# Performance work log

Hardware: AMD Instinct MI355X
Metric: run time of the kernel (lower is better)

## Reference

```python
import jax, jax.numpy as jnp
import numpy as np

LAYERS = [2, 1024, 512, 256, 128, 1]
LB = jnp.array([0.0, 0.0], dtype=jnp.float32)
UB = jnp.array([2.0 * np.pi, 1.0], dtype=jnp.float32)


def _block_diag_mask(num_blocks, bs1, bs2):
    return jnp.kron(jnp.eye(num_blocks, dtype=jnp.float32), jnp.ones((bs1, bs2), jnp.float32))


def _masks():
    # masks for l in range(2, num_Layers - 2) with num_Layers = len(LAYERS) = 6 -> l in {2, 3}
    width = [LAYERS[0]] + [(2 ** (i - 1)) * LAYERS[i] for i in range(1, len(LAYERS) - 1)] + [LAYERS[-1]]
    masks = []
    for l in range(2, len(LAYERS) - 2):
        num_blocks = 2 ** (l - 1)
        bs1 = width[l] // num_blocks
        bs2 = 2 * LAYERS[l + 1]
        masks.append(_block_diag_mask(num_blocks, bs1, bs2))
    return masks


def setup_inputs() -> dict:
    key = jax.random.key(0)
    ks = jax.random.split(key, 8)
    N = 65536
    H = 1024

    def xavier(k, fi, fo):
        lim = float(np.sqrt(6.0 / (fi + fo)))
        return jax.random.uniform(k, (fi, fo), jnp.float32, -lim, lim)

    X = jax.random.uniform(ks[0], (N, 2), jnp.float32, 0.0, 1.0) * (UB - LB) + LB
    return {
        "X": X,
        "W0": xavier(ks[1], 2, H), "b0": jnp.zeros((1, H), jnp.float32),
        "W1": xavier(ks[2], H, H), "b1": jnp.zeros((1, H), jnp.float32),
        "W2": xavier(ks[3], H, H), "b2": jnp.zeros((1, H), jnp.float32),
        "W3": xavier(ks[4], H, H), "b3": jnp.zeros((1, H), jnp.float32),
        "W_last": xavier(ks[5], H, 1), "b_last": jnp.zeros((1, 1), jnp.float32),
    }


def reference(X, W0, b0, W1, b1, W2, b2, W3, b3, W_last, b_last):
    mask2, mask3 = _masks()
    # input normalization to [-1, 1]
    h = 2.0 * (X - LB) / (UB - LB) - 1.0
    h = jnp.tanh(h @ W0 + b0)                 # layer 0: dense
    h = jnp.tanh(h @ W1 + b1)                 # layer 1: dense (no mask in forward)
    h = jnp.tanh(h @ (W2 * mask2) + b2)       # layer 2: block-diagonal masked
    h = jnp.tanh(h @ (W3 * mask3) + b3)       # layer 3: block-diagonal masked
    return h @ W_last + b_last                # output layer, [N, 1]
```

## Files before the change

### kernel.cpp

```cpp
#include <hip/hip_runtime.h>
#include <cstdint>
#include <cstddef>


typedef _Float16  f16x8   __attribute__((ext_vector_type(8)));
typedef float     floatx4 __attribute__((ext_vector_type(4)));
typedef float     floatx8 __attribute__((ext_vector_type(8)));

__device__ __forceinline__ float tanh_fast(float x) {
    float e = __expf(2.0f * x);
    return 1.0f - 2.0f / (e + 1.0f);
}

__global__ __launch_bounds__(256)
void transposeH(const float* __restrict__ W, _Float16* __restrict__ Wt) {
    __shared__ float tile[32][33];
    const int tx = threadIdx.x & 31;
    const int ty = threadIdx.x >> 5;
    #pragma unroll
    for (int j = 0; j < 4; ++j) {
        int r = ty + j * 8;
        tile[r][tx] = W[(size_t)(blockIdx.y * 32 + r) * 1024 + blockIdx.x * 32 + tx];
    }
    __syncthreads();
    #pragma unroll
    for (int j = 0; j < 4; ++j) {
        int r = ty + j * 8;
        Wt[(size_t)(blockIdx.x * 32 + r) * 1024 + blockIdx.y * 32 + tx] =
            (_Float16)tile[tx][r];
    }
}

__global__ __launch_bounds__(256)
void layer0_kernel(const float* __restrict__ X, const float* __restrict__ W0,
                   const float* __restrict__ b0, _Float16* __restrict__ H) {
    const int idx = blockIdx.x * 256 + threadIdx.x;
    const int row = idx >> 7;
    const int j0  = (idx & 127) << 3;
    const float x0 = X[row * 2 + 0];
    const float x1 = X[row * 2 + 1];
    const float xa = x0 * 0.31830988618379067f - 1.0f;
    const float xb = 2.0f * x1 - 1.0f;
    floatx8 wa = *(const floatx8*)(W0 + j0);
    floatx8 wb = *(const floatx8*)(W0 + 1024 + j0);
    floatx8 bb = *(const floatx8*)(b0 + j0);
    f16x8 o;
    #pragma unroll
    for (int j = 0; j < 8; ++j) {
        float v = fmaf(xa, wa[j], fmaf(xb, wb[j], bb[j]));
        o[j] = (_Float16)tanh_fast(v);
    }
    *(f16x8*)(H + (size_t)row * 1024 + j0) = o;
}

__global__ __launch_bounds__(256)
void gemm_tanh_f16(const _Float16* __restrict__ A, const _Float16* __restrict__ Bt,
                   const float* __restrict__ bias, _Float16* __restrict__ C, int KB) {
    __shared__ _Float16 As[128 * 32];
    __shared__ _Float16 Bs[128 * 32];

    const int tid  = threadIdx.x;
    const int lane = tid & 63;
    const int wave = tid >> 6;
    const int m0 = blockIdx.x * 128;
    const int n0 = blockIdx.y * 128;
    const int kbeg   = (n0 / KB) * KB;
    const int kiters = KB >> 5;
    const int wm = (wave & 1) << 6;
    const int wn = (wave >> 1) << 6;
    const int r = lane & 15;
    const int q = lane >> 4;

    const int rowS0 = tid >> 2;
    const int rowS1 = 64 + rowS0;
    const int seg   = (tid & 3) << 3;
    const size_t gA0 = (size_t)(m0 + rowS0) * 1024 + kbeg + seg;
    const size_t gA1 = (size_t)(m0 + rowS1) * 1024 + kbeg + seg;
    const size_t gB0 = (size_t)(n0 + rowS0) * 1024 + kbeg + seg;
    const size_t gB1 = (size_t)(n0 + rowS1) * 1024 + kbeg + seg;
    const int ldsE0 = tid * 8;
    const int ldsE1 = (256 + tid) * 8;

    floatx4 acc[4][4];
    #pragma unroll
    for (int i = 0; i < 4; ++i)
        #pragma unroll
        for (int j = 0; j < 4; ++j)
            acc[i][j] = floatx4{0.f, 0.f, 0.f, 0.f};

    f16x8 va[2], vb[2];
    va[0] = *(const f16x8*)(A + gA0);   va[1] = *(const f16x8*)(A + gA1);
    vb[0] = *(const f16x8*)(Bt + gB0);  vb[1] = *(const f16x8*)(Bt + gB1);

    for (int t = 0; t < kiters; ++t) {
        __syncthreads();
        *(f16x8*)(As + ldsE0) = va[0];  *(f16x8*)(As + ldsE1) = va[1];
        *(f16x8*)(Bs + ldsE0) = vb[0];  *(f16x8*)(Bs + ldsE1) = vb[1];
        __syncthreads();

        if (t + 1 < kiters) {
            const size_t d = (size_t)(t + 1) << 5;
            va[0] = *(const f16x8*)(A + gA0 + d);   va[1] = *(const f16x8*)(A + gA1 + d);
            vb[0] = *(const f16x8*)(Bt + gB0 + d);  vb[1] = *(const f16x8*)(Bt + gB1 + d);
        }

        f16x8 af[4], bf[4];
        #pragma unroll
        for (int i = 0; i < 4; ++i) {
            af[i] = *(const f16x8*)(As + (wm + i * 16 + r) * 32 + q * 8);
            bf[i] = *(const f16x8*)(Bs + (wn + i * 16 + r) * 32 + q * 8);
        }
        #pragma unroll
        for (int i = 0; i < 4; ++i)
            #pragma unroll
            for (int j = 0; j < 4; ++j)
                acc[i][j] = __builtin_amdgcn_mfma_f32_16x16x32_f16(af[i], bf[j], acc[i][j], 0, 0, 0);
    }

    #pragma unroll
    for (int j = 0; j < 4; ++j) {
        const int col = n0 + wn + j * 16 + r;
        const float bv = bias[col];
        #pragma unroll
        for (int i = 0; i < 4; ++i) {
            const int row0 = m0 + wm + i * 16 + q * 4;
            #pragma unroll
            for (int rr = 0; rr < 4; ++rr) {
                float o = tanh_fast(acc[i][j][rr] + bv);
                C[(size_t)(row0 + rr) * 1024 + col] = (_Float16)o;
            }
        }
    }
}

__global__ __launch_bounds__(256)
void final_kernel(const _Float16* __restrict__ H,
                  const float* __restrict__ Wl, const float* __restrict__ bl,
                  float* __restrict__ out) {
    const int lane = threadIdx.x & 63;
    const int wave = threadIdx.x >> 6;
    const int row  = blockIdx.x * 4 + wave;
    const size_t base = (size_t)row * 1024;
    float s = 0.0f;
    #pragma unroll
    for (int c = 0; c < 2; ++c) {
        const int e = c * 512 + lane * 8;
        f16x8 hv = *(const f16x8*)(H + base + e);
        floatx8 wv = *(const floatx8*)(Wl + e);
        #pragma unroll
        for (int j = 0; j < 8; ++j)
            s = fmaf((float)hv[j], wv[j], s);
    }
    #pragma unroll
    for (int off = 32; off > 0; off >>= 1) s += __shfl_down(s, off);
    if (lane == 0) out[row] = s + bl[0];
}

extern "C" void kernel_launch(void* const* d_in, const int* in_sizes, int n_in,
                              void* d_out, int out_size, void* d_ws, size_t ws_size,
                              hipStream_t stream) {
    const float* X  = (const float*)d_in[0];
    const float* W0 = (const float*)d_in[1];
    const float* b0 = (const float*)d_in[2];
    const float* W1 = (const float*)d_in[3];
    const float* b1 = (const float*)d_in[4];
    const float* W2 = (const float*)d_in[5];
    const float* b2 = (const float*)d_in[6];
    const float* W3 = (const float*)d_in[7];
    const float* b3 = (const float*)d_in[8];
    const float* Wl = (const float*)d_in[9];
    const float* bl = (const float*)d_in[10];
    float* out = (float*)d_out;

    const int Nrows = in_sizes[0] / 2;
    const size_t WT = 1024 * 1024;
    const size_t wt_bytes = 3 * WT * 2;
    const size_t slack = 512;

    int R = 0;
    const int Rcap = Nrows < 32768 ? Nrows : 32768;
    for (int r = Rcap; r >= 128; r >>= 1)
        if ((size_t)2 * r * 2048 + wt_bytes + slack <= ws_size) { R = r; break; }
    if (!R) return;

    _Float16* wsp = (_Float16*)d_ws;
    _Float16* Wt1 = wsp;
    _Float16* Wt2 = Wt1 + WT;
    _Float16* Wt3 = Wt2 + WT;
    const size_t plane = (size_t)R * 1024;
    _Float16* P0 = Wt3 + WT;
    _Float16* P1 = P0 + plane;

    const dim3 tb(256);
    transposeH<<<dim3(32, 32), tb, 0, stream>>>(W1, Wt1);
    transposeH<<<dim3(32, 32), tb, 0, stream>>>(W2, Wt2);
    transposeH<<<dim3(32, 32), tb, 0, stream>>>(W3, Wt3);

    const int nchunks = Nrows / R;
    for (int c = 0; c < nchunks; ++c) {
        const float* Xc = X + (size_t)c * R * 2;
        float* outc = out + (size_t)c * R;

        layer0_kernel<<<R / 2, tb, 0, stream>>>(Xc, W0, b0, P0);

        const dim3 gg(R / 128, 8);
        gemm_tanh_f16<<<gg, tb, 0, stream>>>(P0, Wt1, b1, P1, 1024);
        gemm_tanh_f16<<<gg, tb, 0, stream>>>(P1, Wt2, b2, P0, 512);
        gemm_tanh_f16<<<gg, tb, 0, stream>>>(P0, Wt3, b3, P1, 256);

        final_kernel<<<R / 4, tb, 0, stream>>>(P1, Wl, bl, outc);
    }
}
```

Baseline: 596.3 us.

## Fuse output layer into last GEMM via atomics and enlarge GEMM tile to 256x128

The final dot-product layer is folded into the epilogue of the third GEMM. Each wave reduces its tanh outputs times W_last across lanes and atomically adds the partial sum into an output pre-initialised with the bias. This avoids writing and rereading the last hidden activation plane and drops one kernel launch per chunk. The GEMM block also grows to 512 threads with a 256x128 tile so each B tile is reused across more rows. The cost is float atomics with non-deterministic summation order and lower occupancy per block.

```diff
diff --git a/kernel.cpp b/kernel.cpp
--- a/kernel.cpp
+++ b/kernel.cpp
@@ -29,6 +29,11 @@
         Wt[(size_t)(blockIdx.x * 32 + r) * 1024 + blockIdx.y * 32 + tx] =
             (_Float16)tile[tx][r];
     }
+}
+
+__global__ __launch_bounds__(256)
+void init_out(float* __restrict__ out, const float* __restrict__ bl) {
+    out[blockIdx.x * 256 + threadIdx.x] = bl[0];
 }
 
 __global__ __launch_bounds__(256)
@@ -53,33 +58,35 @@
     *(f16x8*)(H + (size_t)row * 1024 + j0) = o;
 }
 
-__global__ __launch_bounds__(256)
+template <bool FUSE>
+__global__ __launch_bounds__(512)
 void gemm_tanh_f16(const _Float16* __restrict__ A, const _Float16* __restrict__ Bt,
-                   const float* __restrict__ bias, _Float16* __restrict__ C, int KB) {
-    __shared__ _Float16 As[128 * 32];
+                   const float* __restrict__ bias, _Float16* __restrict__ C,
+                   const float* __restrict__ Wl, float* __restrict__ out, int KB) {
+    __shared__ _Float16 As[256 * 32];
     __shared__ _Float16 Bs[128 * 32];
 
     const int tid  = threadIdx.x;
     const int lane = tid & 63;
     const int wave = tid >> 6;
-    const int m0 = blockIdx.x * 128;
+    const int m0 = blockIdx.x * 256;
     const int n0 = blockIdx.y * 128;
     const int kbeg   = (n0 / KB) * KB;
     const int kiters = KB >> 5;
-    const int wm = (wave & 1) << 6;
-    const int wn = (wave >> 1) << 6;
+    const int wm = (wave & 3) << 6;
+    const int wn = (wave >> 2) << 6;
     const int r = lane & 15;
     const int q = lane >> 4;
 
-    const int rowS0 = tid >> 2;
-    const int rowS1 = 64 + rowS0;
+    const int rowA0 = tid >> 2;
+    const int rowA1 = 128 + rowA0;
     const int seg   = (tid & 3) << 3;
-    const size_t gA0 = (size_t)(m0 + rowS0) * 1024 + kbeg + seg;
-    const size_t gA1 = (size_t)(m0 + rowS1) * 1024 + kbeg + seg;
-    const size_t gB0 = (size_t)(n0 + rowS0) * 1024 + kbeg + seg;
-    const size_t gB1 = (size_t)(n0 + rowS1) * 1024 + kbeg + seg;
-    const int ldsE0 = tid * 8;
-    const int ldsE1 = (256 + tid) * 8;
+    const size_t gA0 = (size_t)(m0 + rowA0) * 1024 + kbeg + seg;
+    const size_t gA1 = (size_t)(m0 + rowA1) * 1024 + kbeg + seg;
+    const size_t gB  = (size_t)(n0 + rowA0) * 1024 + kbeg + seg;
+    const int ldsA0 = tid * 8;
+    const int ldsA1 = (512 + tid) * 8;
+    const int ldsB  = tid * 8;
 
     floatx4 acc[4][4];
     #pragma unroll
@@ -88,20 +95,22 @@
         for (int j = 0; j < 4; ++j)
             acc[i][j] = floatx4{0.f, 0.f, 0.f, 0.f};
 
-    f16x8 va[2], vb[2];
-    va[0] = *(const f16x8*)(A + gA0);   va[1] = *(const f16x8*)(A + gA1);
-    vb[0] = *(const f16x8*)(Bt + gB0);  vb[1] = *(const f16x8*)(Bt + gB1);
+    f16x8 va0 = *(const f16x8*)(A + gA0);
+    f16x8 va1 = *(const f16x8*)(A + gA1);
+    f16x8 vb  = *(const f16x8*)(Bt + gB);
 
     for (int t = 0; t < kiters; ++t) {
         __syncthreads();
-        *(f16x8*)(As + ldsE0) = va[0];  *(f16x8*)(As + ldsE1) = va[1];
-        *(f16x8*)(Bs + ldsE0) = vb[0];  *(f16x8*)(Bs + ldsE1) = vb[1];
+        *(f16x8*)(As + ldsA0) = va0;
+        *(f16x8*)(As + ldsA1) = va1;
+        *(f16x8*)(Bs + ldsB)  = vb;
         __syncthreads();
 
         if (t + 1 < kiters) {
             const size_t d = (size_t)(t + 1) << 5;
-            va[0] = *(const f16x8*)(A + gA0 + d);   va[1] = *(const f16x8*)(A + gA1 + d);
-            vb[0] = *(const f16x8*)(Bt + gB0 + d);  vb[1] = *(const f16x8*)(Bt + gB1 + d);
+            va0 = *(const f16x8*)(A + gA0 + d);
+            va1 = *(const f16x8*)(A + gA1 + d);
+            vb  = *(const f16x8*)(Bt + gB + d);
         }
 
         f16x8 af[4], bf[4];
@@ -117,43 +126,38 @@
                 acc[i][j] = __builtin_amdgcn_mfma_f32_16x16x32_f16(af[i], bf[j], acc[i][j], 0, 0, 0);
     }
 
+    float bv[4], wlv[4];
     #pragma unroll
     for (int j = 0; j < 4; ++j) {
         const int col = n0 + wn + j * 16 + r;
-        const float bv = bias[col];
-        #pragma unroll
-        for (int i = 0; i < 4; ++i) {
-            const int row0 = m0 + wm + i * 16 + q * 4;
-            #pragma unroll
-            for (int rr = 0; rr < 4; ++rr) {
-                float o = tanh_fast(acc[i][j][rr] + bv);
-                C[(size_t)(row0 + rr) * 1024 + col] = (_Float16)o;
+        bv[j] = bias[col];
+        if (FUSE) wlv[j] = Wl[col];
+    }
+    #pragma unroll
+    for (int i = 0; i < 4; ++i) {
+        const int row0 = m0 + wm + i * 16 + q * 4;
+        #pragma unroll
+        for (int rr = 0; rr < 4; ++rr) {
+            if (!FUSE) {
+                #pragma unroll
+                for (int j = 0; j < 4; ++j) {
+                    float o = tanh_fast(acc[i][j][rr] + bv[j]);
+                    const int col = n0 + wn + j * 16 + r;
+                    C[(size_t)(row0 + rr) * 1024 + col] = (_Float16)o;
+                }
+            } else {
+                float p = 0.f;
+                #pragma unroll
+                for (int j = 0; j < 4; ++j)
+                    p = fmaf(tanh_fast(acc[i][j][rr] + bv[j]), wlv[j], p);
+                p += __shfl_down(p, 8);
+                p += __shfl_down(p, 4);
+                p += __shfl_down(p, 2);
+                p += __shfl_down(p, 1);
+                if (r == 0) atomicAdd(out + row0 + rr, p);
             }
         }
     }
-}
-
-__global__ __launch_bounds__(256)
-void final_kernel(const _Float16* __restrict__ H,
-                  const float* __restrict__ Wl, const float* __restrict__ bl,
-                  float* __restrict__ out) {
-    const int lane = threadIdx.x & 63;
-    const int wave = threadIdx.x >> 6;
-    const int row  = blockIdx.x * 4 + wave;
-    const size_t base = (size_t)row * 1024;
-    float s = 0.0f;
-    #pragma unroll
-    for (int c = 0; c < 2; ++c) {
-        const int e = c * 512 + lane * 8;
-        f16x8 hv = *(const f16x8*)(H + base + e);
-        floatx8 wv = *(const floatx8*)(Wl + e);
-        #pragma unroll
-        for (int j = 0; j < 8; ++j)
-            s = fmaf((float)hv[j], wv[j], s);
-    }
-    #pragma unroll
-    for (int off = 32; off > 0; off >>= 1) s += __shfl_down(s, off);
-    if (lane == 0) out[row] = s + bl[0];
 }
 
 extern "C" void kernel_launch(void* const* d_in, const int* in_sizes, int n_in,
@@ -179,7 +183,7 @@
 
     int R = 0;
     const int Rcap = Nrows < 32768 ? Nrows : 32768;
-    for (int r = Rcap; r >= 128; r >>= 1)
+    for (int r = Rcap; r >= 256; r >>= 1)
         if ((size_t)2 * r * 2048 + wt_bytes + slack <= ws_size) { R = r; break; }
     if (!R) return;
 
@@ -195,6 +199,7 @@
     transposeH<<<dim3(32, 32), tb, 0, stream>>>(W1, Wt1);
     transposeH<<<dim3(32, 32), tb, 0, stream>>>(W2, Wt2);
     transposeH<<<dim3(32, 32), tb, 0, stream>>>(W3, Wt3);
+    init_out<<<Nrows / 256, tb, 0, stream>>>(out, bl);
 
     const int nchunks = Nrows / R;
     for (int c = 0; c < nchunks; ++c) {
@@ -203,11 +208,10 @@
 
         layer0_kernel<<<R / 2, tb, 0, stream>>>(Xc, W0, b0, P0);
 
-        const dim3 gg(R / 128, 8);
-        gemm_tanh_f16<<<gg, tb, 0, stream>>>(P0, Wt1, b1, P1, 1024);
-        gemm_tanh_f16<<<gg, tb, 0, stream>>>(P1, Wt2, b2, P0, 512);
-        gemm_tanh_f16<<<gg, tb, 0, stream>>>(P0, Wt3, b3, P1, 256);
-
-        final_kernel<<<R / 4, tb, 0, stream>>>(P1, Wl, bl, outc);
-    }
-}
+        const dim3 tg(512);
+        const dim3 gg(R / 256, 8);
+        gemm_tanh_f16<false><<<gg, tg, 0, stream>>>(P0, Wt1, b1, P1, nullptr, nullptr, 1024);
+        gemm_tanh_f16<false><<<gg, tg, 0, stream>>>(P1, Wt2, b2, P0, nullptr, nullptr, 512);
+        gemm_tanh_f16<true ><<<gg, tg, 0, stream>>>(P0, Wt3, b3, nullptr, Wl, outc, 256);
+    }
+}
```

Result: faster. 496.0 us (-16.8%).
